# Kernel tuning notes

Hardware: AMD Instinct MI355X
Metric: run time of the kernel (lower is better)

## Reference

```python
import jax, jax.numpy as jnp
import numpy as np

B, N, C = 32, 197, 768   # batch, tokens (num_patches+1), emb_dim
KW = 197                 # kw_dim = seq_len
L = 12                   # num_layers (weights shared, norms per-layer)
HID = 3072               # mlp hidden = 4*emb_dim


def layer_norm(x, g, b, eps=1e-5):
    mu = jnp.mean(x, axis=-1, keepdims=True)
    var = jnp.var(x, axis=-1, keepdims=True)
    return (x - mu) * jax.lax.rsqrt(var + eps) * g + b


def attention(x, qkv_w, fc_w, fc_b, ln_g, ln_b, fc2_w, fc2_b, num_heads):
    b, n, c = x.shape
    d = c // num_heads
    qkv = (x @ qkv_w).reshape(b, n, 3, num_heads, d)
    q = qkv[:, :, 0].transpose(0, 2, 1, 3)  # [B,H,N,d]
    k = qkv[:, :, 1].transpose(0, 2, 1, 3)
    v = qkv[:, :, 2].transpose(0, 2, 1, 3)
    scale = d ** -0.5
    attn = jnp.einsum('bhnd,bhmd->bhnm', q, k) * scale      # [B,H,N,N]
    attn = attn @ fc_w + fc_b                                # [B,H,N,KW]
    attn = layer_norm(attn, ln_g, ln_b)
    attn = jax.nn.softmax(attn, axis=-1)
    attn = attn.transpose(0, 1, 3, 2)                        # [B,H,KW,N]
    y = jnp.einsum('bhkn,bhnd->bhkd', attn, v)               # [B,H,KW,d]
    # fc2 applied along KW axis of y.transpose(-2,-1): out[b,h,n,d]
    out = jnp.einsum('bhkd,kn->bnhd', y, fc2_w) + fc2_b[None, :, None, None]
    return out.reshape(b, n, c)


def mlp(x, w1, b1, w2, b2):
    return jax.nn.gelu(x @ w1 + b1, approximate=False) @ w2 + b2


def setup_inputs() -> dict:
    key = jax.random.key(0)
    ks = jax.random.split(key, 16)
    s = 0.02
    return {
        'x': jax.random.normal(ks[0], (B, N, C), jnp.float32),
        'qkv_w': jax.random.normal(ks[1], (C, 3 * C), jnp.float32) * s,
        'fc_w': jax.random.normal(ks[2], (N, KW), jnp.float32) * s,
        'fc_b': jnp.zeros((KW,), jnp.float32),
        'attn_ln_g': jnp.ones((KW,), jnp.float32),
        'attn_ln_b': jnp.zeros((KW,), jnp.float32),
        'fc2_w': jax.random.normal(ks[3], (KW, N), jnp.float32) * s,
        'fc2_b': jnp.zeros((N,), jnp.float32),
        'mlp_w1': jax.random.normal(ks[4], (C, HID), jnp.float32) * s,
        'mlp_b1': jnp.zeros((HID,), jnp.float32),
        'mlp_w2': jax.random.normal(ks[5], (HID, C), jnp.float32) * s,
        'mlp_b2': jnp.zeros((C,), jnp.float32),
        'f_ln_g': jnp.ones((L, C), jnp.float32),
        'f_ln_b': jnp.zeros((L, C), jnp.float32),
        'g_ln_g': jnp.ones((L, C), jnp.float32),
        'g_ln_b': jnp.zeros((L, C), jnp.float32),
        'num_heads': 12,
    }


def reference(x, qkv_w, fc_w, fc_b, attn_ln_g, attn_ln_b, fc2_w, fc2_b,
              mlp_w1, mlp_b1, mlp_w2, mlp_b2, f_ln_g, f_ln_b, g_ln_g, g_ln_b,
              num_heads):
    # x -> cat([x,x]) -> reversible stack -> mean of the two halves
    x1, x2 = x, x
    n_layers = f_ln_g.shape[0]
    for i in range(n_layers):
        # y1 = x1 + f(x2); y2 = x2 + g(y1)  (PreNorm wraps f and g)
        y1 = x1 + attention(layer_norm(x2, f_ln_g[i], f_ln_b[i]),
                            qkv_w, fc_w, fc_b, attn_ln_g, attn_ln_b,
                            fc2_w, fc2_b, num_heads)
        y2 = x2 + mlp(layer_norm(y1, g_ln_g[i], g_ln_b[i]),
                      mlp_w1, mlp_b1, mlp_w2, mlp_b2)
        x1, x2 = y1, y2
    return (x1 + x2) * 0.5
```

## Files before the change

kernel.cpp:

```cpp
#include <hip/hip_runtime.h>
#include <math.h>

#define BB   32
#define NN   197
#define CC   768
#define HH   12
#define DD   64
#define KWW  197
#define HIDD 3072
#define NL   12
#define RR   (BB*NN)
#define BHH  (BB*HH)
#define NP   224
#define SLS  232

typedef __attribute__((ext_vector_type(8))) short short8;
typedef __attribute__((ext_vector_type(4))) float floatx4;
typedef __attribute__((ext_vector_type(4))) unsigned short us4;

__device__ __forceinline__ unsigned short f2bf(float f) {
    unsigned int u = __float_as_uint(f);
    u += 0x7fff + ((u >> 16) & 1);
    return (unsigned short)(u >> 16);
}

__global__ void ln768_kernel(const float* __restrict__ in, const float* __restrict__ g,
                             const float* __restrict__ be, unsigned short* __restrict__ out) {
    int row = blockIdx.x;
    const float* x = in + (size_t)row * CC;
    unsigned short* o = out + (size_t)row * CC;
    int t = threadIdx.x;
    float v0 = x[t], v1 = x[t+256], v2 = x[t+512];
    float s = v0+v1+v2;
    float q = v0*v0+v1*v1+v2*v2;
    for (int off = 1; off < 64; off <<= 1) {
        s += __shfl_xor(s, off, 64);
        q += __shfl_xor(q, off, 64);
    }
    __shared__ float sh[8];
    int wv = t >> 6, ln = t & 63;
    if (ln == 0) { sh[wv] = s; sh[4+wv] = q; }
    __syncthreads();
    s = sh[0]+sh[1]+sh[2]+sh[3];
    q = sh[4]+sh[5]+sh[6]+sh[7];
    float mu  = s * (1.0f/CC);
    float var = q * (1.0f/CC) - mu*mu;
    float rs  = rsqrtf(var + 1e-5f);
    o[t]     = f2bf((v0-mu)*rs*g[t]     + be[t]);
    o[t+256] = f2bf((v1-mu)*rs*g[t+256] + be[t+256]);
    o[t+512] = f2bf((v2-mu)*rs*g[t+512] + be[t+512]);
}

__global__ void init_ln(const float* __restrict__ x, float* __restrict__ x1,
                        float* __restrict__ x2,
                        const float* __restrict__ g, const float* __restrict__ be,
                        unsigned short* __restrict__ out) {
    int row = blockIdx.x;
    const float* xp = x + (size_t)row * CC;
    int t = threadIdx.x;
    float v0 = xp[t], v1 = xp[t+256], v2 = xp[t+512];
    float* a = x1 + (size_t)row * CC;
    float* b = x2 + (size_t)row * CC;
    a[t] = v0; a[t+256] = v1; a[t+512] = v2;
    b[t] = v0; b[t+256] = v1; b[t+512] = v2;
    float s = v0+v1+v2;
    float q = v0*v0+v1*v1+v2*v2;
    for (int off = 1; off < 64; off <<= 1) {
        s += __shfl_xor(s, off, 64);
        q += __shfl_xor(q, off, 64);
    }
    __shared__ float sh[8];
    int wv = t >> 6, ln = t & 63;
    if (ln == 0) { sh[wv] = s; sh[4+wv] = q; }
    __syncthreads();
    s = sh[0]+sh[1]+sh[2]+sh[3];
    q = sh[4]+sh[5]+sh[6]+sh[7];
    float mu  = s * (1.0f/CC);
    float var = q * (1.0f/CC) - mu*mu;
    float rs  = rsqrtf(var + 1e-5f);
    unsigned short* o = out + (size_t)row * CC;
    o[t]     = f2bf((v0-mu)*rs*g[t]     + be[t]);
    o[t+256] = f2bf((v1-mu)*rs*g[t+256] + be[t+256]);
    o[t+512] = f2bf((v2-mu)*rs*g[t+512] + be[t+512]);
}

__global__ void reduce_ln(float* __restrict__ x2, const float* __restrict__ part,
                          const float* __restrict__ b2,
                          const float* __restrict__ g, const float* __restrict__ be,
                          unsigned short* __restrict__ out,
                          const float* __restrict__ x1f, float* __restrict__ outf,
                          int mode) {
    int row = blockIdx.x;
    float* xp = x2 + (size_t)row * CC;
    const float* p0 = part + (size_t)row * CC;
    const float* p1 = part + (size_t)RR*CC + (size_t)row * CC;
    int t = threadIdx.x;
    float v0 = xp[t]     + p0[t]     + p1[t]     + b2[t];
    float v1 = xp[t+256] + p0[t+256] + p1[t+256] + b2[t+256];
    float v2 = xp[t+512] + p0[t+512] + p1[t+512] + b2[t+512];
    xp[t] = v0; xp[t+256] = v1; xp[t+512] = v2;
    if (mode == 2) {
        const float* xo = x1f + (size_t)row * CC;
        float* o = outf + (size_t)row * CC;
        o[t]     = 0.5f*(xo[t]     + v0);
        o[t+256] = 0.5f*(xo[t+256] + v1);
        o[t+512] = 0.5f*(xo[t+512] + v2);
        return;
    }
    float s = v0+v1+v2;
    float q = v0*v0+v1*v1+v2*v2;
    for (int off = 1; off < 64; off <<= 1) {
        s += __shfl_xor(s, off, 64);
        q += __shfl_xor(q, off, 64);
    }
    __shared__ float sh[8];
    int wv = t >> 6, ln = t & 63;
    if (ln == 0) { sh[wv] = s; sh[4+wv] = q; }
    __syncthreads();
    s = sh[0]+sh[1]+sh[2]+sh[3];
    q = sh[4]+sh[5]+sh[6]+sh[7];
    float mu  = s * (1.0f/CC);
    float var = q * (1.0f/CC) - mu*mu;
    float rs  = rsqrtf(var + 1e-5f);
    unsigned short* o = out + (size_t)row * CC;
    o[t]     = f2bf((v0-mu)*rs*g[t]     + be[t]);
    o[t+256] = f2bf((v1-mu)*rs*g[t+256] + be[t+256]);
    o[t+512] = f2bf((v2-mu)*rs*g[t+512] + be[t+512]);
}

__global__ void transpose_cast(const float* __restrict__ in, unsigned short* __restrict__ out,
                               int K, int Nd, int Kpad) {
    __shared__ float tile[32][33];
    int n0 = blockIdx.x*32, k0 = blockIdx.y*32;
    int tx = threadIdx.x & 31, ty = threadIdx.x >> 5;
    #pragma unroll
    for (int i = 0; i < 4; i++) {
        int k = k0 + ty + i*8;
        tile[ty + i*8][tx] = (k < K && n0+tx < Nd) ? in[(size_t)k*Nd + n0 + tx] : 0.f;
    }
    __syncthreads();
    #pragma unroll
    for (int i = 0; i < 4; i++) {
        int n = n0 + ty + i*8;
        if (n < Nd && k0 + tx < Kpad) out[(size_t)n*Kpad + k0 + tx] = f2bf(tile[tx][ty + i*8]);
    }
}

template<int EPI, int KS>
__global__ __launch_bounds__(256) void gemm128(
    const unsigned short* __restrict__ A, const unsigned short* __restrict__ Bt,
    const float* __restrict__ bias, float* __restrict__ Cf, unsigned short* __restrict__ Cb,
    int M, int Nd, int K)
{
    __shared__ unsigned short As[128*64];
    __shared__ unsigned short Bs[128*64];
    int tid  = threadIdx.x;
    int wv   = tid >> 6, lane = tid & 63;
    int wm   = wv >> 1, wn = wv & 1;
    int quad = lane >> 4, mrow = lane & 15;
    int rl   = lane >> 3, ps = lane & 7;

    int gx   = gridDim.x;
    int nwg  = gx * gridDim.y;
    int orig = blockIdx.y * gx + blockIdx.x;
    int qq = nwg >> 3, rr = nwg & 7;
    int xcd = orig & 7, idx = orig >> 3;
    int wg  = (xcd < rr ? xcd*(qq+1) : rr*(qq+1) + (xcd-rr)*qq) + idx;
    int bm  = (wg / gx) * 128;
    int bn  = (wg % gx) * 128;

    const int Kc    = K / KS;
    const int kbase = (KS > 1) ? blockIdx.z * Kc : 0;

    floatx4 acc[4][4];
    #pragma unroll
    for (int i = 0; i < 4; i++)
        #pragma unroll
        for (int j = 0; j < 4; j++) acc[i][j] = (floatx4){0.f,0.f,0.f,0.f};

    for (int k0 = kbase; k0 < kbase + Kc; k0 += 64) {
        #pragma unroll
        for (int i = 0; i < 4; i++) {
            int r_ = wv*32 + i*8 + rl;
            int sl = ps ^ (r_ & 7);
            int gr = bm + r_; if (gr > M-1) gr = M-1;
            __builtin_amdgcn_global_load_lds(
                (const __attribute__((address_space(1))) void*)(A + (size_t)gr*K + k0 + sl*8),
                (__attribute__((address_space(3))) void*)(As + (wv*32 + i*8)*64),
                16, 0, 0);
        }
        #pragma unroll
        for (int i = 0; i < 4; i++) {
            int r_ = wv*32 + i*8 + rl;
            int sl = ps ^ (r_ & 7);
            int gr = bn + r_;
            __builtin_amdgcn_global_load_lds(
                (const __attribute__((address_space(1))) void*)(Bt + (size_t)gr*K + k0 + sl*8),
                (__attribute__((address_space(3))) void*)(Bs + (wv*32 + i*8)*64),
                16, 0, 0);
        }
        __syncthreads();
        #pragma unroll
        for (int kk = 0; kk < 2; kk++) {
            short8 af[4], bf[4];
            #pragma unroll
            for (int mi = 0; mi < 4; mi++) {
                int lr = wm*64 + mi*16 + mrow;
                af[mi] = *(const short8*)&As[lr*64 + (((kk<<2)|quad) ^ (lr & 7))*8];
            }
            #pragma unroll
            for (int ni = 0; ni < 4; ni++) {
                int lr = wn*64 + ni*16 + mrow;
                bf[ni] = *(const short8*)&Bs[lr*64 + (((kk<<2)|quad) ^ (lr & 7))*8];
            }
            #pragma unroll
            for (int mi = 0; mi < 4; mi++)
                #pragma unroll
                for (int ni = 0; ni < 4; ni++)
                    acc[mi][ni] = __builtin_amdgcn_mfma_f32_16x16x32_bf16(
                        af[mi], bf[ni], acc[mi][ni], 0, 0, 0);
        }
        __syncthreads();
    }

    float* Cfz = (EPI == 5) ? (Cf + (size_t)blockIdx.z * M * Nd) : Cf;
    #pragma unroll
    for (int mi = 0; mi < 4; mi++) {
        int row0 = bm + wm*64 + mi*16 + quad*4;
        #pragma unroll
        for (int ni = 0; ni < 4; ni++) {
            int col = bn + wn*64 + ni*16 + mrow;
            float bv = (EPI == 2) ? bias[col] : 0.f;
            #pragma unroll
            for (int r = 0; r < 4; r++) {
                int row = row0 + r;
                if (row >= M) continue;
                float v = acc[mi][ni][r] + bv;
                if (EPI == 2) {
                    v = v / (1.0f + __expf(-1.5957691216f*v*(1.0f + 0.044715f*v*v)));
                    Cb[(size_t)row*Nd + col] = f2bf(v);
                } else if (EPI == 5) {
                    Cfz[(size_t)row*Nd + col] = v;
                } else if (EPI == 4) {
                    int sel = col / CC;
                    int rem = col - sel*CC;
                    int h = rem >> 6, d = rem & 63;
                    int b = row / NN, n = row - b*NN;
                    int bh = b*HH + h;
                    unsigned short val = f2bf(v);
                    if (sel < 2)
                        Cb[((size_t)sel*BHH + bh)*NN*DD + (size_t)n*DD + d] = val;
                    else
                        Cb[(size_t)2*BHH*NN*DD + (size_t)bh*DD*NP + (size_t)d*NP + n] = val;
                }
            }
        }
    }
}

__global__ __launch_bounds__(256) void attn_score(
    const unsigned short* __restrict__ qb,
    const unsigned short* __restrict__ kb,
    const unsigned short* __restrict__ fw,
    const float* __restrict__ fbias,
    const float* __restrict__ g, const float* __restrict__ be,
    unsigned short* __restrict__ PT)
{
    int bh = blockIdx.y;
    int bm = blockIdx.x * 64;
    __shared__ unsigned short Ks[224*DD];
    __shared__ unsigned short S1s[64*SLS];
    __shared__ float gls[NP], bls[NP], bbs[NP];
    int tid = threadIdx.x;
    if (tid < NP) {
        bool vc = tid < KWW;
        gls[tid] = vc ? g[tid]     : 1.f;
        bls[tid] = vc ? be[tid]    : 0.f;
        bbs[tid] = vc ? fbias[tid] : 0.f;
    }
    int wv = tid >> 6, lane = tid & 63;
    int quad = lane >> 4, mrow = lane & 15;

    {
        int lrow = lane >> 3, lko = (lane & 7) * 8;
        #pragma unroll
        for (int i = 0; i < 7; i++) {
            int r = wv*56 + i*8 + lrow;
            __builtin_amdgcn_global_load_lds(
                (const __attribute__((address_space(1))) void*)(kb + ((size_t)bh*NN + r)*DD + lko),
                (__attribute__((address_space(3))) void*)(Ks + (size_t)(wv*56 + i*8)*DD),
                16, 0, 0);
        }
    }
    int qrow = bm + wv*16 + mrow; if (qrow > NN-1) qrow = NN-1;
    short8 aq0 = *(const short8*)&qb[((size_t)bh*NN + qrow)*DD + quad*8];
    short8 aq1 = *(const short8*)&qb[((size_t)bh*NN + qrow)*DD + 32 + quad*8];
    __syncthreads();

    #pragma unroll
    for (int ni = 0; ni < 14; ni++) {
        floatx4 a = (floatx4){0.f,0.f,0.f,0.f};
        short8 bf0 = *(const short8*)&Ks[(size_t)(ni*16 + mrow)*DD + quad*8];
        short8 bf1 = *(const short8*)&Ks[(size_t)(ni*16 + mrow)*DD + 32 + quad*8];
        a = __builtin_amdgcn_mfma_f32_16x16x32_bf16(aq0, bf0, a, 0, 0, 0);
        a = __builtin_amdgcn_mfma_f32_16x16x32_bf16(aq1, bf1, a, 0, 0, 0);
        #pragma unroll
        for (int r = 0; r < 4; r++)
            S1s[(size_t)(wv*16 + quad*4 + r)*SLS + ni*16 + mrow] = f2bf(a[r]*0.125f);
    }
    __syncthreads();

    floatx4 acc[14];
    #pragma unroll
    for (int j = 0; j < 14; j++) acc[j] = (floatx4){0.f,0.f,0.f,0.f};
    short8 afv[7];
    #pragma unroll
    for (int k0 = 0; k0 < 7; k0++)
        afv[k0] = *(const short8*)&S1s[(size_t)(wv*16 + mrow)*SLS + k0*32 + quad*8];
    #pragma unroll
    for (int k0 = 0; k0 < 7; k0++) {
        #pragma unroll
        for (int ni = 0; ni < 14; ni++) {
            short8 bf = *(const short8*)&fw[(size_t)(ni*16 + mrow)*NP + k0*32 + quad*8];
            acc[ni] = __builtin_amdgcn_mfma_f32_16x16x32_bf16(afv[k0], bf, acc[ni], 0, 0, 0);
        }
    }

    float s[4] = {}, q[4] = {};
    #pragma unroll
    for (int ni = 0; ni < 14; ni++) {
        int col = ni*16 + mrow;
        float cm = (col < KWW) ? 1.f : 0.f;
        #pragma unroll
        for (int r = 0; r < 4; r++) {
            float x = acc[ni][r] + bbs[col];
            acc[ni][r] = x;
            s[r] += x*cm; q[r] += x*x*cm;
        }
    }
    #pragma unroll
    for (int o = 1; o < 16; o <<= 1)
        #pragma unroll
        for (int r = 0; r < 4; r++) {
            s[r] += __shfl_xor(s[r], o, 64);
            q[r] += __shfl_xor(q[r], o, 64);
        }
    float mu[4], rs[4], mx[4];
    #pragma unroll
    for (int r = 0; r < 4; r++) {
        mu[r] = s[r] * (1.0f/KWW);
        float var = q[r] * (1.0f/KWW) - mu[r]*mu[r];
        rs[r] = rsqrtf(var + 1e-5f);
        mx[r] = -1e30f;
    }
    #pragma unroll
    for (int ni = 0; ni < 14; ni++) {
        int col = ni*16 + mrow;
        bool vc = col < KWW;
        #pragma unroll
        for (int r = 0; r < 4; r++) {
            float x = (acc[ni][r] - mu[r]) * rs[r] * gls[col] + bls[col];
            acc[ni][r] = x;
            if (vc) mx[r] = fmaxf(mx[r], x);
        }
    }
    #pragma unroll
    for (int o = 1; o < 16; o <<= 1)
        #pragma unroll
        for (int r = 0; r < 4; r++)
            mx[r] = fmaxf(mx[r], __shfl_xor(mx[r], o, 64));
    float se[4] = {};
    #pragma unroll
    for (int ni = 0; ni < 14; ni++) {
        int col = ni*16 + mrow;
        float cm = (col < KWW) ? 1.f : 0.f;
        #pragma unroll
        for (int r = 0; r < 4; r++) {
            float p = __expf(acc[ni][r] - mx[r]) * cm;
            acc[ni][r] = p;
            se[r] += p;
        }
    }
    #pragma unroll
    for (int o = 1; o < 16; o <<= 1)
        #pragma unroll
        for (int r = 0; r < 4; r++)
            se[r] += __shfl_xor(se[r], o, 64);
    unsigned short* Pb = PT + (size_t)bh*NP*NP;
    int row0 = bm + wv*16 + quad*4;
    float inv0 = 1.0f/se[0], inv1 = 1.0f/se[1], inv2 = 1.0f/se[2], inv3 = 1.0f/se[3];
    #pragma unroll
    for (int ni = 0; ni < 14; ni++) {
        int col = ni*16 + mrow;
        if (col >= KWW) continue;
        if (row0 + 3 < NN) {
            us4 o = { f2bf(acc[ni][0]*inv0), f2bf(acc[ni][1]*inv1),
                      f2bf(acc[ni][2]*inv2), f2bf(acc[ni][3]*inv3) };
            *(us4*)&Pb[(size_t)col*NP + row0] = o;
        } else {
            float invs[4] = {inv0, inv1, inv2, inv3};
            #pragma unroll
            for (int r = 0; r < 4; r++)
                if (row0 + r < NN)
                    Pb[(size_t)col*NP + row0 + r] = f2bf(acc[ni][r]*invs[r]);
        }
    }
}

__global__ __launch_bounds__(256) void attn_out2(
    const unsigned short* __restrict__ PT,
    const unsigned short* __restrict__ vT,
    const unsigned short* __restrict__ fw,
    const float* __restrict__ bias,
    float* __restrict__ x1)
{
    int dt = blockIdx.x;
    int bh = blockIdx.y; int b = bh / HH, h = bh - b*HH;
    __shared__ unsigned short yT[16*232];
    int wv = threadIdx.x >> 6, lane = threadIdx.x & 63;
    int quad = lane >> 4, mrow = lane & 15;
    const unsigned short* Pb = PT + (size_t)bh*NP*NP;
    const unsigned short* Vb = vT + (size_t)bh*DD*NP + (size_t)(dt*16)*NP;

    short8 bfv[7];
    #pragma unroll
    for (int kc = 0; kc < 7; kc++)
        bfv[kc] = *(const short8*)&Vb[(size_t)mrow*NP + kc*32 + quad*8];
    #pragma unroll
    for (int i = 0; i < 2; i++) {
        int t0 = wv + i*8, t1 = t0 + 4;
        bool v1 = t1 < 14;
        floatx4 a0 = (floatx4){0.f,0.f,0.f,0.f};
        floatx4 a1 = (floatx4){0.f,0.f,0.f,0.f};
        #pragma unroll
        for (int kc = 0; kc < 7; kc++) {
            short8 p0 = *(const short8*)&Pb[(size_t)(t0*16 + mrow)*NP + kc*32 + quad*8];
            a0 = __builtin_amdgcn_mfma_f32_16x16x32_bf16(p0, bfv[kc], a0, 0, 0, 0);
            if (v1) {
                short8 p1 = *(const short8*)&Pb[(size_t)(t1*16 + mrow)*NP + kc*32 + quad*8];
                a1 = __builtin_amdgcn_mfma_f32_16x16x32_bf16(p1, bfv[kc], a1, 0, 0, 0);
            }
        }
        us4 o0 = { f2bf(a0[0]), f2bf(a0[1]), f2bf(a0[2]), f2bf(a0[3]) };
        *(us4*)&yT[mrow*232 + t0*16 + quad*4] = o0;
        if (v1) {
            us4 o1 = { f2bf(a1[0]), f2bf(a1[1]), f2bf(a1[2]), f2bf(a1[3]) };
            *(us4*)&yT[mrow*232 + t1*16 + quad*4] = o1;
        }
    }
    __syncthreads();

    short8 yf[7];
    #pragma unroll
    for (int kc = 0; kc < 7; kc++)
        yf[kc] = *(const short8*)&yT[mrow*232 + kc*32 + quad*8];
    float* xb = x1 + (size_t)b*NN*CC + (size_t)h*DD + dt*16 + mrow;
    #pragma unroll
    for (int i = 0; i < 2; i++) {
        int n0t = wv + i*8, n1t = n0t + 4;
        bool v1 = n1t < 13;
        floatx4 a0 = (floatx4){0.f,0.f,0.f,0.f};
        floatx4 a1 = (floatx4){0.f,0.f,0.f,0.f};
        #pragma unroll
        for (int kc = 0; kc < 7; kc++) {
            short8 f0 = *(const short8*)&fw[(size_t)(n0t*16 + mrow)*NP + kc*32 + quad*8];
            a0 = __builtin_amdgcn_mfma_f32_16x16x32_bf16(f0, yf[kc], a0, 0, 0, 0);
            if (v1) {
                short8 f1 = *(const short8*)&fw[(size_t)(n1t*16 + mrow)*NP + kc*32 + quad*8];
                a1 = __builtin_amdgcn_mfma_f32_16x16x32_bf16(f1, yf[kc], a1, 0, 0, 0);
            }
        }
        #pragma unroll
        for (int r = 0; r < 4; r++) {
            int n = n0t*16 + quad*4 + r;
            if (n < NN) xb[(size_t)n*CC] += a0[r] + bias[n];
        }
        if (v1) {
            #pragma unroll
            for (int r = 0; r < 4; r++) {
                int n = n1t*16 + quad*4 + r;
                if (n < NN) xb[(size_t)n*CC] += a1[r] + bias[n];
            }
        }
    }
}

extern "C" void kernel_launch(void* const* d_in, const int* in_sizes, int n_in,
                              void* d_out, int out_size, void* d_ws, size_t ws_size,
                              hipStream_t stream) {
    const float* x     = (const float*)d_in[0];
    const float* qkv_w = (const float*)d_in[1];
    const float* fc_w  = (const float*)d_in[2];
    const float* fc_b  = (const float*)d_in[3];
    const float* alng  = (const float*)d_in[4];
    const float* alnb  = (const float*)d_in[5];
    const float* fc2w  = (const float*)d_in[6];
    const float* fc2b  = (const float*)d_in[7];
    const float* w1    = (const float*)d_in[8];
    const float* b1    = (const float*)d_in[9];
    const float* w2    = (const float*)d_in[10];
    const float* b2    = (const float*)d_in[11];
    const float* flng  = (const float*)d_in[12];
    const float* flnb  = (const float*)d_in[13];
    const float* glng  = (const float*)d_in[14];
    const float* glnb  = (const float*)d_in[15];
    float* out = (float*)d_out;

    float* ws = (float*)d_ws;
    size_t off = 0;
    float* x1 = ws + off; off += (size_t)RR*CC;
    float* x2 = ws + off; off += (size_t)RR*CC;
    float* part = ws + off; off += (size_t)2*RR*CC;
    unsigned short* lnb = (unsigned short*)(ws + off); off += (size_t)RR*CC/2;
    unsigned short* qkvo = (unsigned short*)(ws + off);
    unsigned short* qb = qkvo;
    unsigned short* kb = qkvo + (size_t)BHH*NN*DD;
    unsigned short* vT = qkvo + (size_t)2*BHH*NN*DD;
    off += ((size_t)2*BHH*NN*DD + (size_t)BHH*DD*NP + 1) / 2;
    unsigned short* PT   = (unsigned short*)(ws + off); off += (size_t)BHH*NP*NP/2;
    unsigned short* hid  = (unsigned short*)(ws + off); off += (size_t)RR*HIDD/2;
    unsigned short* qkv_wt = (unsigned short*)(ws + off); off += (size_t)3*CC*CC/2;
    unsigned short* w1t    = (unsigned short*)(ws + off); off += (size_t)CC*HIDD/2;
    unsigned short* w2t    = (unsigned short*)(ws + off); off += (size_t)CC*HIDD/2;
    unsigned short* fc_wt  = (unsigned short*)(ws + off); off += (size_t)NP*NP/2 + 16;
    unsigned short* fc2_wt = (unsigned short*)(ws + off); off += (size_t)NP*NP/2 + 16;

    hipMemsetAsync(vT, 0, (size_t)BHH*DD*NP*2, stream);
    hipMemsetAsync(fc_wt, 0, (size_t)NP*NP*2, stream);
    hipMemsetAsync(fc2_wt, 0, (size_t)NP*NP*2, stream);

    transpose_cast<<<dim3(72, 24), 256, 0, stream>>>(qkv_w, qkv_wt, CC, 3*CC, CC);
    transpose_cast<<<dim3(96, 24), 256, 0, stream>>>(w1, w1t, CC, HIDD, CC);
    transpose_cast<<<dim3(24, 96), 256, 0, stream>>>(w2, w2t, HIDD, CC, HIDD);
    transpose_cast<<<dim3(7, 7),   256, 0, stream>>>(fc_w,  fc_wt,  NN, KWW, NP);
    transpose_cast<<<dim3(7, 7),   256, 0, stream>>>(fc2w,  fc2_wt, KWW, NN, NP);

    init_ln<<<RR, 256, 0, stream>>>(x, x1, x2, flng, flnb, lnb);

    const int MT = (RR + 127) / 128;
    for (int l = 0; l < NL; l++) {
        gemm128<4,1><<<dim3(3*CC/128, MT), 256, 0, stream>>>(
            lnb, qkv_wt, nullptr, nullptr, qb, RR, 3*CC, CC);
        attn_score<<<dim3(4, BHH), 256, 0, stream>>>(
            qb, kb, fc_wt, fc_b, alng, alnb, PT);
        attn_out2<<<dim3(4, BHH), 256, 0, stream>>>(PT, vT, fc2_wt, fc2b, x1);
        ln768_kernel<<<RR, 256, 0, stream>>>(x1, glng + l*CC, glnb + l*CC, lnb);
        gemm128<2,1><<<dim3(HIDD/128, MT), 256, 0, stream>>>(
            lnb, w1t, b1, nullptr, hid, RR, HIDD, CC);
        gemm128<5,2><<<dim3(CC/128, MT, 2), 256, 0, stream>>>(
            hid, w2t, nullptr, part, nullptr, RR, CC, HIDD);
        if (l + 1 < NL) {
            reduce_ln<<<RR, 256, 0, stream>>>(
                x2, part, b2, flng + (l+1)*CC, flnb + (l+1)*CC, lnb,
                nullptr, nullptr, 1);
        } else {
            reduce_ln<<<RR, 256, 0, stream>>>(
                x2, part, b2, nullptr, nullptr, nullptr, x1, out, 2);
        }
    }
}
```

Measured before the change: 3.619 ms.

## Stage fc_w tiles in LDS and XOR-swizzle K and fc_w shared layouts

In the attention score kernel, the fc weight operand is now streamed into a shared-memory tile per k-step with async global-to-LDS loads, instead of every wave reading it directly from global memory. K rows in LDS are also XOR-swizzled to reduce bank conflicts on the MFMA operand reads. The aim is to cut redundant global/L2 traffic for fc_w and LDS bank conflicts. In exchange it adds two barriers per k-step, about 14KB more LDS (which may lower occupancy), and drops the prefetched A-fragment registers.

```diff
diff --git a/kernel.cpp b/kernel.cpp
--- a/kernel.cpp
+++ b/kernel.cpp
@@ -270,6 +270,7 @@
     int bm = blockIdx.x * 64;
     __shared__ unsigned short Ks[224*DD];
     __shared__ unsigned short S1s[64*SLS];
+    __shared__ unsigned short Bs[224*32];
     __shared__ float gls[NP], bls[NP], bbs[NP];
     int tid = threadIdx.x;
     if (tid < NP) {
@@ -282,10 +283,11 @@
     int quad = lane >> 4, mrow = lane & 15;
 
     {
-        int lrow = lane >> 3, lko = (lane & 7) * 8;
+        int lrow = lane >> 3, lsl = lane & 7;
         #pragma unroll
         for (int i = 0; i < 7; i++) {
             int r = wv*56 + i*8 + lrow;
+            int lko = (lsl ^ (r & 7)) * 8;
             __builtin_amdgcn_global_load_lds(
                 (const __attribute__((address_space(1))) void*)(kb + ((size_t)bh*NN + r)*DD + lko),
                 (__attribute__((address_space(3))) void*)(Ks + (size_t)(wv*56 + i*8)*DD),
@@ -300,8 +302,9 @@
     #pragma unroll
     for (int ni = 0; ni < 14; ni++) {
         floatx4 a = (floatx4){0.f,0.f,0.f,0.f};
-        short8 bf0 = *(const short8*)&Ks[(size_t)(ni*16 + mrow)*DD + quad*8];
-        short8 bf1 = *(const short8*)&Ks[(size_t)(ni*16 + mrow)*DD + 32 + quad*8];
+        int lr = ni*16 + mrow;
+        short8 bf0 = *(const short8*)&Ks[(size_t)lr*DD + ((quad    ) ^ (lr & 7))*8];
+        short8 bf1 = *(const short8*)&Ks[(size_t)lr*DD + ((4 + quad) ^ (lr & 7))*8];
         a = __builtin_amdgcn_mfma_f32_16x16x32_bf16(aq0, bf0, a, 0, 0, 0);
         a = __builtin_amdgcn_mfma_f32_16x16x32_bf16(aq1, bf1, a, 0, 0, 0);
         #pragma unroll
@@ -313,17 +316,25 @@
     floatx4 acc[14];
     #pragma unroll
     for (int j = 0; j < 14; j++) acc[j] = (floatx4){0.f,0.f,0.f,0.f};
-    short8 afv[7];
-    #pragma unroll
-    for (int k0 = 0; k0 < 7; k0++)
-        afv[k0] = *(const short8*)&S1s[(size_t)(wv*16 + mrow)*SLS + k0*32 + quad*8];
-    #pragma unroll
     for (int k0 = 0; k0 < 7; k0++) {
+        for (int c = wv; c < 14; c += 4) {
+            int r_ = c*16 + (lane >> 2);
+            int gr = r_; if (gr > KWW-1) gr = KWW-1;
+            int sl = ((lane & 3) ^ (r_ & 3)) * 8;
+            __builtin_amdgcn_global_load_lds(
+                (const __attribute__((address_space(1))) void*)(fw + (size_t)gr*NP + k0*32 + sl),
+                (__attribute__((address_space(3))) void*)(Bs + (size_t)(c*16)*32),
+                16, 0, 0);
+        }
+        __syncthreads();
+        short8 af = *(const short8*)&S1s[(size_t)(wv*16 + mrow)*SLS + k0*32 + quad*8];
         #pragma unroll
         for (int ni = 0; ni < 14; ni++) {
-            short8 bf = *(const short8*)&fw[(size_t)(ni*16 + mrow)*NP + k0*32 + quad*8];
-            acc[ni] = __builtin_amdgcn_mfma_f32_16x16x32_bf16(afv[k0], bf, acc[ni], 0, 0, 0);
-        }
+            int lr = ni*16 + mrow;
+            short8 bf = *(const short8*)&Bs[(size_t)lr*32 + (quad ^ (lr & 3))*8];
+            acc[ni] = __builtin_amdgcn_mfma_f32_16x16x32_bf16(af, bf, acc[ni], 0, 0, 0);
+        }
+        __syncthreads();
     }
 
     float s[4] = {}, q[4] = {};
```

Result: faster. 3.351 ms (-7.4%).
